# Kernel optimization log

Hardware: AMD Instinct MI355X
Metric: run time of the kernel (lower is better)

The kernel has to match this reference:

```python
import jax, jax.numpy as jnp
import numpy as np

TEMPERATURE = 1.0
EPS = 1e-5
COS_EPS = 1e-8  # torch CosineSimilarity default eps
N_POS, N_NEG, D = 512, 512, 512


def setup_inputs() -> dict:
    key = jax.random.key(0)
    k1, k2, k3 = jax.random.split(key, 3)
    tensor_positive = jax.random.normal(k1, (N_POS, D), dtype=jnp.float32)
    tensor_negative = jax.random.normal(k2, (N_NEG, D), dtype=jnp.float32)
    # nn.Linear(512*3, 1), weight ~ N(0, 0.02^2), bias zeros
    linear_w = jax.random.normal(k3, (1, 3 * D), dtype=jnp.float32) * 0.02
    linear_b = jnp.zeros((1,), dtype=jnp.float32)
    return {"tensor_positive": tensor_positive, "tensor_negative": tensor_negative,
            "linear_w": linear_w, "linear_b": linear_b}


def _cos_matrix(a, b):
    # pairwise cosine similarity [Na, Nb], matching torch CosineSimilarity eps clamp
    an = a / jnp.maximum(jnp.linalg.norm(a, axis=-1, keepdims=True), COS_EPS)
    bn = b / jnp.maximum(jnp.linalg.norm(b, axis=-1, keepdims=True), COS_EPS)
    return an @ bn.T


def reference(tensor_positive, tensor_negative, linear_w, linear_b):
    pos, neg = tensor_positive, tensor_negative
    n_pos, d = pos.shape
    n_neg = neg.shape[0]

    # NCE part
    logit_n = jnp.exp(_cos_matrix(pos, neg) / TEMPERATURE)        # [N, M]
    deno_n = jnp.sum(logit_n, axis=-1)                            # [N]
    logit_p = jnp.exp(_cos_matrix(pos, pos) / TEMPERATURE)        # [N, N]
    loss = jnp.sum(-jnp.log(logit_p / (deno_n[:, None] + logit_p + EPS)))

    # Pairwise classifier: linear(cat([a, b, |a-b|])) decomposed as
    # a@w1 + b@w2 + |a-b|@w3 to avoid materializing the 3D concat.
    w = linear_w[0]
    w1, w2, w3 = w[:d], w[d:2 * d], w[2 * d:]
    allv = jnp.concatenate([pos, neg], axis=0)                    # [N+M, D]
    t1 = pos @ w1                                                 # [N]
    t2 = allv @ w2                                                # [N+M]
    diff = jnp.abs(pos[:, None, :] - allv[None, :, :])            # [N, N+M, D]
    t3 = jnp.einsum('nmd,d->nm', diff, w3)                        # [N, N+M]
    logits = t1[:, None] + t2[None, :] + t3 + linear_b[0]
    labels = jnp.concatenate([jnp.ones((n_pos,), jnp.float32),
                              jnp.zeros((n_neg,), jnp.float32)])  # [N+M]
    # BCE(sigmoid(logits), labels), stable form; per-i mean then sum over i
    bce = labels[None, :] * jax.nn.softplus(-logits) + (1.0 - labels[None, :]) * jax.nn.softplus(logits)
    loss = loss + jnp.sum(jnp.mean(bce, axis=1))
    return loss
```

## Files before the change

### kernel.cpp

```cpp
#include <hip/hip_runtime.h>
#include <math.h>

#define NPOS 512
#define DIM  512
#define NB   1024
#define EPSV 1e-5f
#define COS_EPS 1e-8f

#define OFF_INV 0
#define OFF_T1  1024
#define OFF_T2  1536
#define OFF_S   2560
#define PSZ     (NPOS * NB)
#define OFF_TP  (OFF_S + PSZ)
#define OFF_BF  (OFF_TP + 8 * PSZ)

#define FSW(x) ((x) + 4 * ((x) >> 5))

typedef __attribute__((ext_vector_type(8))) __bf16 bf16x8;
typedef __attribute__((ext_vector_type(4))) float  f32x4;

__device__ __forceinline__ float softplus_f(float x) {
    return fmaxf(x, 0.f) + __logf(1.f + __expf(-fabsf(x)));
}

__device__ __forceinline__ unsigned short f2bf(float f) {
    union { float f; unsigned int u; } v; v.f = f;
    unsigned int r = (v.u + 0x7fffu + ((v.u >> 16) & 1u)) >> 16;
    return (unsigned short)r;
}

__global__ __launch_bounds__(256) void prep_kernel(
    const float* __restrict__ pos, const float* __restrict__ neg,
    const float* __restrict__ w, float* __restrict__ ws, float* __restrict__ out)
{
    int gtid = blockIdx.x * 256 + threadIdx.x;
    if (gtid == 0) out[0] = 0.f;
    int row  = gtid >> 6;
    int lane = threadIdx.x & 63;
    if (row >= NB) return;
    bool is_pos = row < NPOS;
    const float* r = is_pos ? pos + row * DIM : neg + (row - NPOS) * DIM;

    const float4* r4  = (const float4*)r + lane * 2;
    const float4* w14 = (const float4*)(w) + lane * 2;
    const float4* w24 = (const float4*)(w + DIM) + lane * 2;
    float4 a0 = r4[0],  a1 = r4[1];
    float4 u0 = w14[0], u1 = w14[1];
    float4 v0 = w24[0], v1 = w24[1];

    uint4 pk;
    pk.x = (unsigned)f2bf(a0.x) | ((unsigned)f2bf(a0.y) << 16);
    pk.y = (unsigned)f2bf(a0.z) | ((unsigned)f2bf(a0.w) << 16);
    pk.z = (unsigned)f2bf(a1.x) | ((unsigned)f2bf(a1.y) << 16);
    pk.w = (unsigned)f2bf(a1.z) | ((unsigned)f2bf(a1.w) << 16);
    ((uint4*)(ws + OFF_BF))[row * 64 + lane] = pk;

    float ss  = a0.x*a0.x + a0.y*a0.y + a0.z*a0.z + a0.w*a0.w
              + a1.x*a1.x + a1.y*a1.y + a1.z*a1.z + a1.w*a1.w;
    float dw1 = a0.x*u0.x + a0.y*u0.y + a0.z*u0.z + a0.w*u0.w
              + a1.x*u1.x + a1.y*u1.y + a1.z*u1.z + a1.w*u1.w;
    float dw2 = a0.x*v0.x + a0.y*v0.y + a0.z*v0.z + a0.w*v0.w
              + a1.x*v1.x + a1.y*v1.y + a1.z*v1.z + a1.w*v1.w;

    #pragma unroll
    for (int off = 32; off; off >>= 1) {
        ss  += __shfl_xor(ss, off);
        dw1 += __shfl_xor(dw1, off);
        dw2 += __shfl_xor(dw2, off);
    }
    if (lane == 0) {
        float inv = 1.f / fmaxf(sqrtf(ss), COS_EPS);
        ws[OFF_INV + row] = inv;
        ws[OFF_T2 + row]  = dw2;
        if (is_pos) ws[OFF_T1 + row] = dw1;
    }
}

__global__ __launch_bounds__(256) void cosmat_mfma(
    float* __restrict__ ws)
{
    const int wave = (blockIdx.x * 256 + threadIdx.x) >> 6;
    const int lane = threadIdx.x & 63;
    const int n0 = (wave >> 6) << 4;
    const int m0 = (wave & 63) << 4;
    const int rc   = lane & 15;
    const int quad = lane >> 4;

    const unsigned short* bf = (const unsigned short*)(ws + OFF_BF);
    const bf16x8* pa = (const bf16x8*)(bf + (n0 + rc) * DIM + quad * 8);
    const bf16x8* pb = (const bf16x8*)(bf + (m0 + rc) * DIM + quad * 8);

    f32x4 acc = {0.f, 0.f, 0.f, 0.f};
    #pragma unroll
    for (int k = 0; k < 16; ++k)
        acc = __builtin_amdgcn_mfma_f32_16x16x32_bf16(pa[4 * k], pb[4 * k], acc, 0, 0, 0);

    float* S = ws + OFF_S;
    const float invm = ws[OFF_INV + m0 + rc];
    #pragma unroll
    for (int e = 0; e < 4; ++e) {
        int n = n0 + quad * 4 + e;
        S[(size_t)n * NB + m0 + rc] = acc[e] * ws[OFF_INV + n] * invm;
    }
}

__global__ __launch_bounds__(256, 2) void t3_kernel(
    const float* __restrict__ pos, const float* __restrict__ neg,
    const float* __restrict__ w, float* __restrict__ ws)
{
    __shared__ __align__(16) float As[64][68];
    __shared__ __align__(16) float Bs[64][140];

    const int tid = threadIdx.x;
    const int m0 = blockIdx.x * 128;
    const int n0 = blockIdx.y * 64;
    const int kb = blockIdx.z * 64;

    const float* Asrc = pos + (size_t)n0 * DIM + kb;
    const float* Bsrc = ((m0 < NPOS) ? (pos + (size_t)m0 * DIM)
                                     : (neg + (size_t)(m0 - NPOS) * DIM)) + kb;
    const float* w3 = w + 2 * DIM + kb;

    {
        const int r = tid >> 2, g = (tid & 3) * 16;
        #pragma unroll
        for (int u = 0; u < 4; ++u) {
            float4 v = *(const float4*)(Asrc + (size_t)r * DIM + g + 4 * u);
            As[g + 4 * u + 0][r] = v.x;
            As[g + 4 * u + 1][r] = v.y;
            As[g + 4 * u + 2][r] = v.z;
            As[g + 4 * u + 3][r] = v.w;
        }
    }
    {
        const int r = tid >> 1, h = (tid & 1) * 32;
        const int fr = FSW(r);
        #pragma unroll
        for (int u = 0; u < 8; ++u) {
            float4 v = *(const float4*)(Bsrc + (size_t)r * DIM + h + 4 * u);
            Bs[h + 4 * u + 0][fr] = v.x;
            Bs[h + 4 * u + 1][fr] = v.y;
            Bs[h + 4 * u + 2][fr] = v.z;
            Bs[h + 4 * u + 3][fr] = v.w;
        }
    }
    __syncthreads();

    const int n4 = (tid & 15) * 4;
    const int m8 = (tid >> 4) * 8;
    const int fm = FSW(m8);

    float acc[4][8] = {{0.f}};

    #pragma unroll 4
    for (int k = 0; k < 64; ++k) {
        const float4 av = *(const float4*)&As[k][n4];
        const float4 b0 = *(const float4*)&Bs[k][fm];
        const float4 b1 = *(const float4*)&Bs[k][fm + 4];
        const float wk = w3[k];
        const float a[4] = {av.x, av.y, av.z, av.w};
        const float b[8] = {b0.x, b0.y, b0.z, b0.w, b1.x, b1.y, b1.z, b1.w};
        #pragma unroll
        for (int r = 0; r < 4; ++r)
            #pragma unroll
            for (int s = 0; s < 8; ++s)
                acc[r][s] = fmaf(fabsf(a[r] - b[s]), wk, acc[r][s]);
    }

    float* Tp = ws + OFF_TP + (size_t)blockIdx.z * PSZ;
    #pragma unroll
    for (int r = 0; r < 4; ++r) {
        int n = n0 + n4 + r;
        float4 o0 = {acc[r][0], acc[r][1], acc[r][2], acc[r][3]};
        float4 o1 = {acc[r][4], acc[r][5], acc[r][6], acc[r][7]};
        *(float4*)(Tp + (size_t)n * NB + m0 + m8)     = o0;
        *(float4*)(Tp + (size_t)n * NB + m0 + m8 + 4) = o1;
    }
}

__global__ __launch_bounds__(256) void finish_kernel(
    const float* __restrict__ lb, const float* __restrict__ ws, float* __restrict__ out)
{
    __shared__ float eneg_s[4];
    __shared__ float red[4];

    const int n  = blockIdx.x;
    const int wv = threadIdx.x >> 6;
    const int l  = threadIdx.x & 63;
    const int i4 = wv * 64 + l;

    const float4 cc = ((const float4*)(ws + OFF_S + (size_t)n * NB))[i4];

    float4 tt = {0.f, 0.f, 0.f, 0.f};
    #pragma unroll
    for (int z = 0; z < 8; ++z) {
        const float4 p = ((const float4*)(ws + OFF_TP + (size_t)z * PSZ + (size_t)n * NB))[i4];
        tt.x += p.x; tt.y += p.y; tt.z += p.z; tt.w += p.w;
    }

    float ep = 0.f;
    if (wv >= 2)
        ep = __expf(cc.x) + __expf(cc.y) + __expf(cc.z) + __expf(cc.w);
    #pragma unroll
    for (int off = 32; off; off >>= 1) ep += __shfl_xor(ep, off);
    if (l == 0) eneg_s[wv] = ep;
    __syncthreads();
    const float eneg = eneg_s[2] + eneg_s[3];

    float part = 0.f;
    if (wv < 2) {
        part += __logf(eneg + __expf(cc.x) + EPSV) - cc.x;
        part += __logf(eneg + __expf(cc.y) + EPSV) - cc.y;
        part += __logf(eneg + __expf(cc.z) + EPSV) - cc.z;
        part += __logf(eneg + __expf(cc.w) + EPSV) - cc.w;
    }

    const float t1n  = ws[OFF_T1 + n];
    const float bias = lb[0];
    const float4 t2 = *(const float4*)(ws + OFF_T2 + 4 * i4);
    float lgx = t1n + t2.x + tt.x + bias;
    float lgy = t1n + t2.y + tt.y + bias;
    float lgz = t1n + t2.z + tt.z + bias;
    float lgw = t1n + t2.w + tt.w + bias;
    float b;
    if (wv < 2)
        b = softplus_f(-lgx) + softplus_f(-lgy) + softplus_f(-lgz) + softplus_f(-lgw);
    else
        b = softplus_f(lgx) + softplus_f(lgy) + softplus_f(lgz) + softplus_f(lgw);
    part += b * (1.f / 1024.f);

    #pragma unroll
    for (int off = 32; off; off >>= 1) part += __shfl_xor(part, off);
    if (l == 0) red[wv] = part;
    __syncthreads();
    if (threadIdx.x == 0)
        atomicAdd(out, red[0] + red[1] + red[2] + red[3]);
}

extern "C" void kernel_launch(void* const* d_in, const int* in_sizes, int n_in,
                              void* d_out, int out_size, void* d_ws, size_t ws_size,
                              hipStream_t stream) {
    (void)in_sizes; (void)n_in; (void)out_size; (void)ws_size;
    const float* pos = (const float*)d_in[0];
    const float* neg = (const float*)d_in[1];
    const float* w   = (const float*)d_in[2];
    const float* lb  = (const float*)d_in[3];
    float* out = (float*)d_out;
    float* ws  = (float*)d_ws;

    prep_kernel<<<256, 256, 0, stream>>>(pos, neg, w, ws, out);
    cosmat_mfma<<<512, 256, 0, stream>>>(ws);
    t3_kernel<<<dim3(8, 8, 8), 256, 0, stream>>>(pos, neg, w, ws);
    finish_kernel<<<512, 256, 0, stream>>>(lb, ws, out);
}
```

Measured before the change: 110.7 us.

## Merge prep, cosine MFMA and t3 kernels into one independent-block launch

Combines the three producer kernels into a single launch where block ranges perform the t3 partial sums, the cosine Gram matrix, or the per-row norm/dot prep. The cosine MFMA now converts fp32 rows to bf16 in registers instead of reading a bf16 copy, and the normalization by inverse norms moves into the finish kernel, which removes the dependency between prep and MFMA. This removes two launches and the bf16 staging buffer, at the cost of redundant bf16 conversion and heavier per-block branching and shared-memory reservation for all blocks.

```diff
diff --git a/kernel.cpp b/kernel.cpp
--- a/kernel.cpp
+++ b/kernel.cpp
@@ -13,7 +13,6 @@
 #define OFF_S   2560
 #define PSZ     (NPOS * NB)
 #define OFF_TP  (OFF_S + PSZ)
-#define OFF_BF  (OFF_TP + 8 * PSZ)
 
 #define FSW(x) ((x) + 4 * ((x) >> 5))
 
@@ -24,158 +23,156 @@
     return fmaxf(x, 0.f) + __logf(1.f + __expf(-fabsf(x)));
 }
 
-__device__ __forceinline__ unsigned short f2bf(float f) {
-    union { float f; unsigned int u; } v; v.f = f;
-    unsigned int r = (v.u + 0x7fffu + ((v.u >> 16) & 1u)) >> 16;
-    return (unsigned short)r;
-}
-
-__global__ __launch_bounds__(256) void prep_kernel(
+__device__ __forceinline__ unsigned f2bf2(float lo, float hi) {
+    union { float f; unsigned u; } a, b; a.f = lo; b.f = hi;
+    unsigned x = (a.u + 0x7fffu + ((a.u >> 16) & 1u)) >> 16;
+    unsigned y = (b.u + 0x7fffu + ((b.u >> 16) & 1u)) >> 16;
+    return x | (y << 16);
+}
+
+__global__ __launch_bounds__(256) void mega_kernel(
     const float* __restrict__ pos, const float* __restrict__ neg,
     const float* __restrict__ w, float* __restrict__ ws, float* __restrict__ out)
 {
-    int gtid = blockIdx.x * 256 + threadIdx.x;
-    if (gtid == 0) out[0] = 0.f;
-    int row  = gtid >> 6;
-    int lane = threadIdx.x & 63;
-    if (row >= NB) return;
-    bool is_pos = row < NPOS;
-    const float* r = is_pos ? pos + row * DIM : neg + (row - NPOS) * DIM;
-
-    const float4* r4  = (const float4*)r + lane * 2;
-    const float4* w14 = (const float4*)(w) + lane * 2;
-    const float4* w24 = (const float4*)(w + DIM) + lane * 2;
-    float4 a0 = r4[0],  a1 = r4[1];
-    float4 u0 = w14[0], u1 = w14[1];
-    float4 v0 = w24[0], v1 = w24[1];
-
-    uint4 pk;
-    pk.x = (unsigned)f2bf(a0.x) | ((unsigned)f2bf(a0.y) << 16);
-    pk.y = (unsigned)f2bf(a0.z) | ((unsigned)f2bf(a0.w) << 16);
-    pk.z = (unsigned)f2bf(a1.x) | ((unsigned)f2bf(a1.y) << 16);
-    pk.w = (unsigned)f2bf(a1.z) | ((unsigned)f2bf(a1.w) << 16);
-    ((uint4*)(ws + OFF_BF))[row * 64 + lane] = pk;
-
-    float ss  = a0.x*a0.x + a0.y*a0.y + a0.z*a0.z + a0.w*a0.w
-              + a1.x*a1.x + a1.y*a1.y + a1.z*a1.z + a1.w*a1.w;
-    float dw1 = a0.x*u0.x + a0.y*u0.y + a0.z*u0.z + a0.w*u0.w
-              + a1.x*u1.x + a1.y*u1.y + a1.z*u1.z + a1.w*u1.w;
-    float dw2 = a0.x*v0.x + a0.y*v0.y + a0.z*v0.z + a0.w*v0.w
-              + a1.x*v1.x + a1.y*v1.y + a1.z*v1.z + a1.w*v1.w;
-
-    #pragma unroll
-    for (int off = 32; off; off >>= 1) {
-        ss  += __shfl_xor(ss, off);
-        dw1 += __shfl_xor(dw1, off);
-        dw2 += __shfl_xor(dw2, off);
-    }
-    if (lane == 0) {
-        float inv = 1.f / fmaxf(sqrtf(ss), COS_EPS);
-        ws[OFF_INV + row] = inv;
-        ws[OFF_T2 + row]  = dw2;
-        if (is_pos) ws[OFF_T1 + row] = dw1;
-    }
-}
-
-__global__ __launch_bounds__(256) void cosmat_mfma(
-    float* __restrict__ ws)
-{
-    const int wave = (blockIdx.x * 256 + threadIdx.x) >> 6;
-    const int lane = threadIdx.x & 63;
-    const int n0 = (wave >> 6) << 4;
-    const int m0 = (wave & 63) << 4;
-    const int rc   = lane & 15;
-    const int quad = lane >> 4;
-
-    const unsigned short* bf = (const unsigned short*)(ws + OFF_BF);
-    const bf16x8* pa = (const bf16x8*)(bf + (n0 + rc) * DIM + quad * 8);
-    const bf16x8* pb = (const bf16x8*)(bf + (m0 + rc) * DIM + quad * 8);
-
-    f32x4 acc = {0.f, 0.f, 0.f, 0.f};
-    #pragma unroll
-    for (int k = 0; k < 16; ++k)
-        acc = __builtin_amdgcn_mfma_f32_16x16x32_bf16(pa[4 * k], pb[4 * k], acc, 0, 0, 0);
-
-    float* S = ws + OFF_S;
-    const float invm = ws[OFF_INV + m0 + rc];
-    #pragma unroll
-    for (int e = 0; e < 4; ++e) {
-        int n = n0 + quad * 4 + e;
-        S[(size_t)n * NB + m0 + rc] = acc[e] * ws[OFF_INV + n] * invm;
-    }
-}
-
-__global__ __launch_bounds__(256, 2) void t3_kernel(
-    const float* __restrict__ pos, const float* __restrict__ neg,
-    const float* __restrict__ w, float* __restrict__ ws)
-{
     __shared__ __align__(16) float As[64][68];
     __shared__ __align__(16) float Bs[64][140];
 
+    const int b   = blockIdx.x;
     const int tid = threadIdx.x;
-    const int m0 = blockIdx.x * 128;
-    const int n0 = blockIdx.y * 64;
-    const int kb = blockIdx.z * 64;
-
-    const float* Asrc = pos + (size_t)n0 * DIM + kb;
-    const float* Bsrc = ((m0 < NPOS) ? (pos + (size_t)m0 * DIM)
-                                     : (neg + (size_t)(m0 - NPOS) * DIM)) + kb;
-    const float* w3 = w + 2 * DIM + kb;
-
-    {
-        const int r = tid >> 2, g = (tid & 3) * 16;
+
+    if (b < 512) {
+        const int z  = b >> 6;
+        const int bb = b & 63;
+        const int n0 = (bb >> 3) * 64;
+        const int m0 = (bb & 7) * 128;
+        const int kb = z * 64;
+
+        const float* Asrc = pos + (size_t)n0 * DIM + kb;
+        const float* Bsrc = ((m0 < NPOS) ? (pos + (size_t)m0 * DIM)
+                                         : (neg + (size_t)(m0 - NPOS) * DIM)) + kb;
+        const float* w3 = w + 2 * DIM + kb;
+
+        {
+            const int r = tid >> 2, g = (tid & 3) * 16;
+            #pragma unroll
+            for (int u = 0; u < 4; ++u) {
+                float4 v = *(const float4*)(Asrc + (size_t)r * DIM + g + 4 * u);
+                As[g + 4 * u + 0][r] = v.x;
+                As[g + 4 * u + 1][r] = v.y;
+                As[g + 4 * u + 2][r] = v.z;
+                As[g + 4 * u + 3][r] = v.w;
+            }
+        }
+        {
+            const int r = tid >> 1, h = (tid & 1) * 32;
+            const int fr = FSW(r);
+            #pragma unroll
+            for (int u = 0; u < 8; ++u) {
+                float4 v = *(const float4*)(Bsrc + (size_t)r * DIM + h + 4 * u);
+                Bs[h + 4 * u + 0][fr] = v.x;
+                Bs[h + 4 * u + 1][fr] = v.y;
+                Bs[h + 4 * u + 2][fr] = v.z;
+                Bs[h + 4 * u + 3][fr] = v.w;
+            }
+        }
+        __syncthreads();
+
+        const int n4 = (tid & 15) * 4;
+        const int m8 = (tid >> 4) * 8;
+        const int fm = FSW(m8);
+
+        float acc[4][8] = {{0.f}};
+
+        #pragma unroll 4
+        for (int k = 0; k < 64; ++k) {
+            const float4 av = *(const float4*)&As[k][n4];
+            const float4 b0 = *(const float4*)&Bs[k][fm];
+            const float4 b1 = *(const float4*)&Bs[k][fm + 4];
+            const float wk = w3[k];
+            const float a[4] = {av.x, av.y, av.z, av.w};
+            const float bv[8] = {b0.x, b0.y, b0.z, b0.w, b1.x, b1.y, b1.z, b1.w};
+            #pragma unroll
+            for (int r = 0; r < 4; ++r)
+                #pragma unroll
+                for (int s = 0; s < 8; ++s)
+                    acc[r][s] = fmaf(fabsf(a[r] - bv[s]), wk, acc[r][s]);
+        }
+
+        float* Tp = ws + OFF_TP + (size_t)z * PSZ;
         #pragma unroll
-        for (int u = 0; u < 4; ++u) {
-            float4 v = *(const float4*)(Asrc + (size_t)r * DIM + g + 4 * u);
-            As[g + 4 * u + 0][r] = v.x;
-            As[g + 4 * u + 1][r] = v.y;
-            As[g + 4 * u + 2][r] = v.z;
-            As[g + 4 * u + 3][r] = v.w;
-        }
-    }
-    {
-        const int r = tid >> 1, h = (tid & 1) * 32;
-        const int fr = FSW(r);
+        for (int r = 0; r < 4; ++r) {
+            int n = n0 + n4 + r;
+            float4 o0 = {acc[r][0], acc[r][1], acc[r][2], acc[r][3]};
+            float4 o1 = {acc[r][4], acc[r][5], acc[r][6], acc[r][7]};
+            *(float4*)(Tp + (size_t)n * NB + m0 + m8)     = o0;
+            *(float4*)(Tp + (size_t)n * NB + m0 + m8 + 4) = o1;
+        }
+    } else if (b < 1024) {
+        const int wave = ((b - 512) << 2) | (tid >> 6);
+        const int lane = tid & 63;
+        const int n0 = (wave >> 6) << 4;
+        const int m0 = (wave & 63) << 4;
+        const int rc   = lane & 15;
+        const int quad = lane >> 4;
+
+        const float* arow = pos + (size_t)(n0 + rc) * DIM + quad * 8;
+        const float* brow = ((m0 < NPOS) ? (pos + (size_t)(m0 + rc) * DIM)
+                                         : (neg + (size_t)(m0 - NPOS + rc) * DIM)) + quad * 8;
+
+        f32x4 acc = {0.f, 0.f, 0.f, 0.f};
+        #pragma unroll 4
+        for (int k = 0; k < 16; ++k) {
+            float4 a0 = *(const float4*)(arow + k * 32);
+            float4 a1 = *(const float4*)(arow + k * 32 + 4);
+            float4 b0 = *(const float4*)(brow + k * 32);
+            float4 b1 = *(const float4*)(brow + k * 32 + 4);
+            union { unsigned u[4]; bf16x8 v; } af, bf;
+            af.u[0] = f2bf2(a0.x, a0.y); af.u[1] = f2bf2(a0.z, a0.w);
+            af.u[2] = f2bf2(a1.x, a1.y); af.u[3] = f2bf2(a1.z, a1.w);
+            bf.u[0] = f2bf2(b0.x, b0.y); bf.u[1] = f2bf2(b0.z, b0.w);
+            bf.u[2] = f2bf2(b1.x, b1.y); bf.u[3] = f2bf2(b1.z, b1.w);
+            acc = __builtin_amdgcn_mfma_f32_16x16x32_bf16(af.v, bf.v, acc, 0, 0, 0);
+        }
+
+        float* S = ws + OFF_S;
         #pragma unroll
-        for (int u = 0; u < 8; ++u) {
-            float4 v = *(const float4*)(Bsrc + (size_t)r * DIM + h + 4 * u);
-            Bs[h + 4 * u + 0][fr] = v.x;
-            Bs[h + 4 * u + 1][fr] = v.y;
-            Bs[h + 4 * u + 2][fr] = v.z;
-            Bs[h + 4 * u + 3][fr] = v.w;
-        }
-    }
-    __syncthreads();
-
-    const int n4 = (tid & 15) * 4;
-    const int m8 = (tid >> 4) * 8;
-    const int fm = FSW(m8);
-
-    float acc[4][8] = {{0.f}};
-
-    #pragma unroll 4
-    for (int k = 0; k < 64; ++k) {
-        const float4 av = *(const float4*)&As[k][n4];
-        const float4 b0 = *(const float4*)&Bs[k][fm];
-        const float4 b1 = *(const float4*)&Bs[k][fm + 4];
-        const float wk = w3[k];
-        const float a[4] = {av.x, av.y, av.z, av.w};
-        const float b[8] = {b0.x, b0.y, b0.z, b0.w, b1.x, b1.y, b1.z, b1.w};
+        for (int e = 0; e < 4; ++e) {
+            int n = n0 + quad * 4 + e;
+            S[(size_t)n * NB + m0 + rc] = acc[e];
+        }
+    } else {
+        if (b == 1024 && tid == 0) out[0] = 0.f;
+        int row  = ((b - 1024) << 2) | (tid >> 6);
+        int lane = tid & 63;
+        bool is_pos = row < NPOS;
+        const float* r = is_pos ? pos + (size_t)row * DIM : neg + (size_t)(row - NPOS) * DIM;
+
+        const float4* r4  = (const float4*)r + lane * 2;
+        const float4* w14 = (const float4*)(w) + lane * 2;
+        const float4* w24 = (const float4*)(w + DIM) + lane * 2;
+        float4 a0 = r4[0],  a1 = r4[1];
+        float4 u0 = w14[0], u1 = w14[1];
+        float4 v0 = w24[0], v1 = w24[1];
+
+        float ss  = a0.x*a0.x + a0.y*a0.y + a0.z*a0.z + a0.w*a0.w
+                  + a1.x*a1.x + a1.y*a1.y + a1.z*a1.z + a1.w*a1.w;
+        float dw1 = a0.x*u0.x + a0.y*u0.y + a0.z*u0.z + a0.w*u0.w
+                  + a1.x*u1.x + a1.y*u1.y + a1.z*u1.z + a1.w*u1.w;
+        float dw2 = a0.x*v0.x + a0.y*v0.y + a0.z*v0.z + a0.w*v0.w
+                  + a1.x*v1.x + a1.y*v1.y + a1.z*v1.z + a1.w*v1.w;
+
         #pragma unroll
-        for (int r = 0; r < 4; ++r)
-            #pragma unroll
-            for (int s = 0; s < 8; ++s)
-                acc[r][s] = fmaf(fabsf(a[r] - b[s]), wk, acc[r][s]);
-    }
-
-    float* Tp = ws + OFF_TP + (size_t)blockIdx.z * PSZ;
-    #pragma unroll
-    for (int r = 0; r < 4; ++r) {
-        int n = n0 + n4 + r;
-        float4 o0 = {acc[r][0], acc[r][1], acc[r][2], acc[r][3]};
-        float4 o1 = {acc[r][4], acc[r][5], acc[r][6], acc[r][7]};
-        *(float4*)(Tp + (size_t)n * NB + m0 + m8)     = o0;
-        *(float4*)(Tp + (size_t)n * NB + m0 + m8 + 4) = o1;
+        for (int off = 32; off; off >>= 1) {
+            ss  += __shfl_xor(ss, off);
+            dw1 += __shfl_xor(dw1, off);
+            dw2 += __shfl_xor(dw2, off);
+        }
+        if (lane == 0) {
+            float inv = 1.f / fmaxf(sqrtf(ss), COS_EPS);
+            ws[OFF_INV + row] = inv;
+            ws[OFF_T2 + row]  = dw2;
+            if (is_pos) ws[OFF_T1 + row] = dw1;
+        }
     }
 }
 
@@ -190,7 +187,14 @@
     const int l  = threadIdx.x & 63;
     const int i4 = wv * 64 + l;
 
-    const float4 cc = ((const float4*)(ws + OFF_S + (size_t)n * NB))[i4];
+    const float invn = ws[OFF_INV + n];
+    const float4 sraw = ((const float4*)(ws + OFF_S + (size_t)n * NB))[i4];
+    const float4 inv4 = *(const float4*)(ws + OFF_INV + 4 * i4);
+    float4 cc;
+    cc.x = sraw.x * invn * inv4.x;
+    cc.y = sraw.y * invn * inv4.y;
+    cc.z = sraw.z * invn * inv4.z;
+    cc.w = sraw.w * invn * inv4.w;
 
     float4 tt = {0.f, 0.f, 0.f, 0.f};
     #pragma unroll
@@ -223,12 +227,12 @@
     float lgy = t1n + t2.y + tt.y + bias;
     float lgz = t1n + t2.z + tt.z + bias;
     float lgw = t1n + t2.w + tt.w + bias;
-    float b;
+    float bb;
     if (wv < 2)
-        b = softplus_f(-lgx) + softplus_f(-lgy) + softplus_f(-lgz) + softplus_f(-lgw);
+        bb = softplus_f(-lgx) + softplus_f(-lgy) + softplus_f(-lgz) + softplus_f(-lgw);
     else
-        b = softplus_f(lgx) + softplus_f(lgy) + softplus_f(lgz) + softplus_f(lgw);
-    part += b * (1.f / 1024.f);
+        bb = softplus_f(lgx) + softplus_f(lgy) + softplus_f(lgz) + softplus_f(lgw);
+    part += bb * (1.f / 1024.f);
 
     #pragma unroll
     for (int off = 32; off; off >>= 1) part += __shfl_xor(part, off);
@@ -249,8 +253,6 @@
     float* out = (float*)d_out;
     float* ws  = (float*)d_ws;
 
-    prep_kernel<<<256, 256, 0, stream>>>(pos, neg, w, ws, out);
-    cosmat_mfma<<<512, 256, 0, stream>>>(ws);
-    t3_kernel<<<dim3(8, 8, 8), 256, 0, stream>>>(pos, neg, w, ws);
+    mega_kernel<<<1280, 256, 0, stream>>>(pos, neg, w, ws, out);
     finish_kernel<<<512, 256, 0, stream>>>(lb, ws, out);
 }
```

After: 107.8 us. 2.6% less time.
